# Optimization experiments

Hardware: AMD Instinct MI355X
Metric: run time of the kernel (lower is better)

Reference implementation:

```python
import jax, jax.numpy as jnp
import numpy as np
from jax import lax

T = 30        # FISTA iterations
C = 64        # number of conv filters
K = 31        # filter length
LAM = 0.1     # sparsity weight
L = 5.0       # Lipschitz constant (step size 1/L)
B, N = 32, 8192


def _HT(r, H):
    # F.conv1d(r, H): r [B,1,N], H [C,1,K] -> [B,C,N-K+1] (cross-correlation, VALID)
    return lax.conv_general_dilated(r, H, (1,), 'VALID',
                                    dimension_numbers=('NCH', 'OIH', 'NCH'))


def _Hop(x, H):
    # F.conv_transpose1d(x, H): x [B,C,M], H [C,1,K] -> [B,1,M+K-1]
    # adjoint of VALID cross-correlation = FULL conv with flipped kernel, I/O swapped
    W = jnp.transpose(jnp.flip(H, -1), (1, 0, 2))  # [1,C,K] in OIH
    return lax.conv_general_dilated(x, W, (1,), [(K - 1, K - 1)],
                                    dimension_numbers=('NCH', 'OIH', 'NCH'))


def setup_inputs() -> dict:
    key = jax.random.key(0)
    k1, k2 = jax.random.split(key)
    y = jax.random.normal(k1, (B, 1, N), dtype=jnp.float32)
    H = jax.random.normal(k2, (C, 1, K), dtype=jnp.float32)
    H = H / jnp.linalg.norm(H, axis=-1, keepdims=True)  # F.normalize(p=2, dim=-1)
    return {"y": y, "H": H}


def reference(y, H):
    enc_dim = y.shape[-1] - K + 1
    Bq = y.shape[0]
    thr = LAM / L
    x0 = jnp.zeros((Bq, C, enc_dim), dtype=y.dtype)
    init = (x0, x0, jnp.float32(1.0))  # x_old, x_tmp, s_old

    def step(carry, _):
        x_old, x_tmp, s_old = carry
        res = y - _Hop(x_tmp, H)
        x_new = jax.nn.relu(x_tmp + _HT(res, H) / L - thr)
        s_new = (1.0 + jnp.sqrt(1.0 + 4.0 * s_old * s_old)) / 2.0
        x_tmp_n = x_new + (s_old - 1.0) / s_new * (x_new - x_old)
        return (x_new, x_tmp_n, s_new), None

    (x_new, _, _), _ = lax.scan(step, init, None, length=T)
    y_hat = _Hop(x_new, H)
    return (y_hat, x_new)
```

## Files before the change

kernel.cpp:

```cpp
#include <hip/hip_runtime.h>
#include <math.h>


#define BB   32
#define CCH  64
#define KF   31
#define NN   8192
#define MM   8162
#define TT   30
#define TILE 256
#define NT   32
#define HS_P 37
#define XS_C 356
#define RACC_P 292

#define BCM ((size_t)BB * CCH * MM)
#define BN  ((size_t)BB * NN)

__device__ __forceinline__ int Fi(int i) { return i + ((i >> 5) << 2); }

__global__ __launch_bounds__(256) void step_kernel(
    const float* __restrict__ y, const float* __restrict__ Hg,
    const float* __restrict__ xA,
    float* __restrict__ xW,
    const float* __restrict__ rcur, float* __restrict__ rnext,
    float* __restrict__ rzero, float c0, float c1)
{
    __shared__ __attribute__((aligned(16))) float Hs[CCH * HS_P];
    __shared__ __attribute__((aligned(16))) float resv[320];
    __shared__ __attribute__((aligned(16))) float xs[16 * XS_C];
    __shared__ __attribute__((aligned(16))) float racc[4 * RACC_P];

    const int tid = threadIdx.x;
    const int m0  = blockIdx.x * TILE;
    const int b   = blockIdx.y;
    const size_t yb = (size_t)b * NN;

    for (int s = tid; s < CCH * HS_P; s += 256) {
        int c = s / HS_P, k = s - c * HS_P;
        Hs[s] = (k < KF) ? Hg[c * KF + k] : 0.f;
    }
    for (int i = tid; i < 288; i += 256) {
        int n = m0 + i; float v = 0.f;
        if (i < 286 && n < NN) v = y[yb + n] - rcur[yb + n];
        resv[Fi(i)] = v;
    }
    for (int s = tid; s < 16 * 64; s += 256) {
        int row = s >> 6, q = s & 63;
        int raw = (q < 32) ? q : (q + 256);
        xs[row * XS_C + Fi(raw)] = 0.f;
    }
    rzero[yb + m0 + tid] = 0.f;
    __syncthreads();

    const int wv    = tid >> 6, lane = tid & 63;
    const int cb2   = lane >> 4, lanem = lane & 15;
    const int ogi   = lane & 31, csi   = lane >> 5;
    const int ib    = ogi * 9;

    float r9[9];
    #pragma unroll
    for (int j = 0; j < 9; ++j) r9[j] = 0.f;

    #pragma unroll 1
    for (int r = 0; r < 4; ++r) {
        {
            const int c = wv * 16 + r * 4 + cb2;
            float* xrow = xs + (wv * 4 + cb2) * XS_C;
            const size_t xg = ((size_t)(b * CCH + c)) * MM;
            const float* hr = Hs + c * HS_P;
            #pragma unroll
            for (int p = 0; p < 2; ++p) {
                const int lb = p * 128 + lanem * 8;
                const int mb = m0 + lb;
                const size_t g = xg + mb;
                const bool fast = (mb + 7 < MM);
                float av[8], bv[8];
                if (fast) {
                    #pragma unroll
                    for (int j = 0; j < 8; j += 2) {
                        float2 t2 = *(const float2*)(xA + g + j);
                        av[j] = t2.x; av[j + 1] = t2.y;
                    }
                    #pragma unroll
                    for (int j = 0; j < 8; j += 2) {
                        float2 t2 = *(const float2*)(xW + g + j);
                        bv[j] = t2.x; bv[j + 1] = t2.y;
                    }
                }
                float w[16];
                #pragma unroll
                for (int q = 0; q < 4; ++q) {
                    float4 qv = *(const float4*)&resv[Fi(lb + 4 * q)];
                    w[4 * q] = qv.x; w[4 * q + 1] = qv.y;
                    w[4 * q + 2] = qv.z; w[4 * q + 3] = qv.w;
                }
                float h4[4];
                #pragma unroll
                for (int i2 = 0; i2 < 4; ++i2) h4[i2] = hr[i2];
                float acc[8];
                #pragma unroll
                for (int j = 0; j < 8; ++j) acc[j] = 0.f;
                #pragma unroll
                for (int kb = 0; kb < 32; kb += 4) {
                    float hn[4];
                    if (kb < 28) {
                        #pragma unroll
                        for (int i2 = 0; i2 < 4; ++i2) hn[i2] = hr[kb + 4 + i2];
                    }
                    float4 rq;
                    if (kb < 24) rq = *(const float4*)&resv[Fi(lb + kb + 16)];
                    #pragma unroll
                    for (int kk = 0; kk < 4; ++kk) {
                        const int k = kb + kk;
                        const float h = h4[kk];
                        #pragma unroll
                        for (int j = 0; j < 8; ++j)
                            acc[j] = fmaf(w[(k + j) & 15], h, acc[j]);
                    }
                    if (kb < 24) {
                        w[(kb + 0) & 15] = rq.x; w[(kb + 1) & 15] = rq.y;
                        w[(kb + 2) & 15] = rq.z; w[(kb + 3) & 15] = rq.w;
                    }
                    if (kb < 28) {
                        #pragma unroll
                        for (int i2 = 0; i2 < 4; ++i2) h4[i2] = hn[i2];
                    }
                }
                if (fast) {
                    float xn[8], x1[8];
                    #pragma unroll
                    for (int j = 0; j < 8; ++j) {
                        float xt = fmaf(c0, av[j] - bv[j], av[j]);
                        xn[j] = fmaxf(fmaf(acc[j], 0.2f, xt) - 0.02f, 0.f);
                        x1[j] = fmaf(c1, xn[j] - av[j], xn[j]);
                    }
                    *(float4*)&xrow[Fi(32 + lb)] =
                        make_float4(x1[0], x1[1], x1[2], x1[3]);
                    *(float4*)&xrow[Fi(32 + lb + 4)] =
                        make_float4(x1[4], x1[5], x1[6], x1[7]);
                    #pragma unroll
                    for (int j = 0; j < 8; j += 2)
                        *(float2*)(xW + g + j) = make_float2(xn[j], xn[j + 1]);
                } else {
                    #pragma unroll
                    for (int j = 0; j < 8; ++j) {
                        float x1 = 0.f;
                        if (mb + j < MM) {
                            float a = xA[g + j], b2 = xW[g + j];
                            float xt = fmaf(c0, a - b2, a);
                            float v  = fmaxf(fmaf(acc[j], 0.2f, xt) - 0.02f, 0.f);
                            xW[g + j] = v;
                            x1 = fmaf(c1, v - a, v);
                        }
                        xrow[Fi(32 + lb + j)] = x1;
                    }
                }
            }
        }

        #pragma unroll
        for (int cc = 0; cc < 2; ++cc) {
            const int cl = 2 * csi + cc;
            const float* xr = xs + (wv * 4 + cl) * XS_C;
            const float* hc = Hs + (wv * 16 + r * 4 + cl) * HS_P;
            float w[16];
            #pragma unroll
            for (int s = 0; s < 16; ++s) w[s] = xr[Fi(32 + ib - 7 + s)];
            float h4[4];
            #pragma unroll
            for (int i2 = 0; i2 < 4; ++i2) h4[i2] = hc[i2];
            #pragma unroll
            for (int kb = 0; kb < 32; kb += 4) {
                float hn[4];
                if (kb < 28) {
                    #pragma unroll
                    for (int i2 = 0; i2 < 4; ++i2) hn[i2] = hc[kb + 4 + i2];
                }
                float rv[4];
                if (kb < 24) {
                    #pragma unroll
                    for (int i2 = 0; i2 < 4; ++i2)
                        rv[i2] = xr[Fi(32 + ib - 8 - (kb + i2))];
                }
                #pragma unroll
                for (int kk = 0; kk < 4; ++kk) {
                    const int k = kb + kk;
                    const float h = h4[kk];
                    #pragma unroll
                    for (int j = 0; j < 9; ++j)
                        r9[j] = fmaf(w[(j - k + 7) & 15], h, r9[j]);
                }
                if (kb < 24) {
                    #pragma unroll
                    for (int i2 = 0; i2 < 4; ++i2)
                        w[(15 - (kb + i2)) & 15] = rv[i2];
                }
                if (kb < 28) {
                    #pragma unroll
                    for (int i2 = 0; i2 < 4; ++i2) h4[i2] = hn[i2];
                }
            }
        }
    }

    #pragma unroll
    for (int j = 0; j < 9; ++j) r9[j] += __shfl_xor(r9[j], 32);
    if (lane < 32) {
        #pragma unroll
        for (int j = 0; j < 9; ++j) racc[wv * RACC_P + ib + j] = r9[j];
    }
    __syncthreads();
    for (int i = tid; i < 286; i += 256) {
        int n = m0 + i;
        if (n < NN) {
            float s4 = racc[i] + racc[RACC_P + i] +
                       racc[2 * RACC_P + i] + racc[3 * RACC_P + i];
            atomicAdd(&rnext[yb + n], s4);
        }
    }
}

extern "C" void kernel_launch(void* const* d_in, const int* in_sizes, int n_in,
                              void* d_out, int out_size, void* d_ws, size_t ws_size,
                              hipStream_t stream) {
    const float* y  = (const float*)d_in[0];
    const float* Hg = (const float*)d_in[1];

    float* out  = (float*)d_out;
    float* yhat = out;
    float* xout = out + BN;
    float* x0w  = (float*)d_ws;
    float* r0   = x0w + BCM;
    float* r1   = r0 + BN;
    float* r2   = r1 + BN;
    float* rb[3] = {r0, r1, r2};

    hipMemsetAsync(x0w, 0, (BCM + 3 * BN) * sizeof(float), stream);
    hipMemsetAsync(out, 0, (BN + BCM) * sizeof(float), stream);

    dim3 grid(NT, BB);
    float s = 1.f, beta_prev = 0.f;
    for (int t = 0; t < TT; ++t) {
        float snew = (1.f + sqrtf(1.f + 4.f * s * s)) * 0.5f;
        float beta = (s - 1.f) / snew;
        float c1v = (t == TT - 1) ? 0.f : beta;
        float* xWt       = (t & 1) ? xout : x0w;
        const float* xAt = (t & 1) ? x0w  : xout;
        float* rnext = (t == TT - 1) ? yhat : rb[(t + 1) % 3];
        step_kernel<<<grid, 256, 0, stream>>>(y, Hg, xAt, xWt,
            rb[t % 3], rnext, rb[(t + 2) % 3], beta_prev, c1v);
        beta_prev = beta;
        s = snew;
    }
}
```

Measured before the change: 2.247 ms.

## Enlarge tile to 384, keep filter taps in registers, restructure transpose conv

The tile grows from 256 to 384 outputs per block, so the grid drops from 32 to 22 tiles per batch and the 30-tap halo overhead shrinks relative to useful work. The filter is stored in a reordered shared layout and loaded once into 32 registers per channel, so both the correlation and the transpose convolution reuse them instead of re-reading shared memory each tap. The transpose conv now has each lane compute 8 outputs for its own channel, then reduces across the four channel lanes with shuffles and accumulates into shared memory, plus a separate tail pass for the halo outputs. The cost is higher register pressure, extra shuffle and shared-memory read-modify-write traffic, and fewer blocks in flight.

```diff
diff --git a/kernel.cpp b/kernel.cpp
--- a/kernel.cpp
+++ b/kernel.cpp
@@ -8,11 +8,11 @@
 #define NN   8192
 #define MM   8162
 #define TT   30
-#define TILE 256
-#define NT   32
-#define HS_P 37
-#define XS_C 356
-#define RACC_P 292
+#define TILE 384
+#define NTI  22
+#define XS_C 500
+#define RV_N 464
+#define RP   464
 
 #define BCM ((size_t)BB * CCH * MM)
 #define BN  ((size_t)BB * NN)
@@ -26,196 +26,201 @@
     const float* __restrict__ rcur, float* __restrict__ rnext,
     float* __restrict__ rzero, float c0, float c1)
 {
-    __shared__ __attribute__((aligned(16))) float Hs[CCH * HS_P];
-    __shared__ __attribute__((aligned(16))) float resv[320];
+    __shared__ __attribute__((aligned(16))) float Hs2[2048];
+    __shared__ __attribute__((aligned(16))) float resv[RV_N];
     __shared__ __attribute__((aligned(16))) float xs[16 * XS_C];
-    __shared__ __attribute__((aligned(16))) float racc[4 * RACC_P];
+    __shared__ __attribute__((aligned(16))) float racc[4 * RP];
 
     const int tid = threadIdx.x;
     const int m0  = blockIdx.x * TILE;
     const int b   = blockIdx.y;
     const size_t yb = (size_t)b * NN;
 
-    for (int s = tid; s < CCH * HS_P; s += 256) {
-        int c = s / HS_P, k = s - c * HS_P;
-        Hs[s] = (k < KF) ? Hg[c * KF + k] : 0.f;
-    }
-    for (int i = tid; i < 288; i += 256) {
+    for (int s = tid; s < 2048; s += 256) {
+        int g = s >> 7, rem = s & 127;
+        int q = rem >> 4, sl = rem & 15;
+        int cb = sl >> 2, e = sl & 3;
+        int c = (g >> 2) * 16 + (g & 3) * 4 + cb;
+        int tap = q * 4 + e;
+        Hs2[s] = (tap < KF) ? Hg[c * KF + tap] : 0.f;
+    }
+    for (int i = tid; i < 416; i += 256) {
         int n = m0 + i; float v = 0.f;
-        if (i < 286 && n < NN) v = y[yb + n] - rcur[yb + n];
+        if (i < 414 && n < NN) v = y[yb + n] - rcur[yb + n];
         resv[Fi(i)] = v;
     }
     for (int s = tid; s < 16 * 64; s += 256) {
         int row = s >> 6, q = s & 63;
-        int raw = (q < 32) ? q : (q + 256);
+        int raw = (q < 32) ? q : (q + 384);
         xs[row * XS_C + Fi(raw)] = 0.f;
     }
-    rzero[yb + m0 + tid] = 0.f;
+    for (int s = tid; s < 4 * RP; s += 256) racc[s] = 0.f;
+    for (int i = tid; i < TILE; i += 256) {
+        int n = m0 + i;
+        if (n < NN) rzero[yb + n] = 0.f;
+    }
     __syncthreads();
 
     const int wv    = tid >> 6, lane = tid & 63;
     const int cb2   = lane >> 4, lanem = lane & 15;
-    const int ogi   = lane & 31, csi   = lane >> 5;
-    const int ib    = ogi * 9;
-
-    float r9[9];
-    #pragma unroll
-    for (int j = 0; j < 9; ++j) r9[j] = 0.f;
 
     #pragma unroll 1
     for (int r = 0; r < 4; ++r) {
+        const int c = wv * 16 + r * 4 + cb2;
+        float* xrow = xs + (wv * 4 + cb2) * XS_C;
+        const size_t xg = ((size_t)(b * CCH + c)) * MM;
+
+        float hv[32];
         {
-            const int c = wv * 16 + r * 4 + cb2;
-            float* xrow = xs + (wv * 4 + cb2) * XS_C;
-            const size_t xg = ((size_t)(b * CCH + c)) * MM;
-            const float* hr = Hs + c * HS_P;
-            #pragma unroll
-            for (int p = 0; p < 2; ++p) {
-                const int lb = p * 128 + lanem * 8;
-                const int mb = m0 + lb;
-                const size_t g = xg + mb;
-                const bool fast = (mb + 7 < MM);
-                float av[8], bv[8];
-                if (fast) {
+            const int hb = (wv * 4 + r) * 128 + cb2 * 4;
+            #pragma unroll
+            for (int q = 0; q < 8; ++q) {
+                float4 t = *(const float4*)&Hs2[hb + q * 16];
+                hv[q*4] = t.x; hv[q*4+1] = t.y; hv[q*4+2] = t.z; hv[q*4+3] = t.w;
+            }
+        }
+
+        #pragma unroll 1
+        for (int p = 0; p < 3; ++p) {
+            const int lb = p * 128 + lanem * 8;
+            const int mb = m0 + lb;
+            const size_t g = xg + mb;
+            const bool fast = (mb + 7 < MM);
+            float av[8], bv[8];
+            if (fast) {
+                #pragma unroll
+                for (int j = 0; j < 8; j += 2) {
+                    float2 t2 = *(const float2*)(xA + g + j);
+                    av[j] = t2.x; av[j + 1] = t2.y;
+                }
+                #pragma unroll
+                for (int j = 0; j < 8; j += 2) {
+                    float2 t2 = *(const float2*)(xW + g + j);
+                    bv[j] = t2.x; bv[j + 1] = t2.y;
+                }
+            }
+            float w[16];
+            #pragma unroll
+            for (int q = 0; q < 4; ++q) {
+                float4 v = *(const float4*)&resv[Fi(lb + 4 * q)];
+                w[4*q] = v.x; w[4*q+1] = v.y; w[4*q+2] = v.z; w[4*q+3] = v.w;
+            }
+            float acc[8];
+            #pragma unroll
+            for (int j = 0; j < 8; ++j) acc[j] = 0.f;
+            #pragma unroll
+            for (int kb = 0; kb < 32; kb += 4) {
+                float4 rq;
+                if (kb <= 20) rq = *(const float4*)&resv[Fi(lb + 16 + kb)];
+                #pragma unroll
+                for (int kk = 0; kk < 4; ++kk) {
+                    const float h = hv[kb + kk];
                     #pragma unroll
-                    for (int j = 0; j < 8; j += 2) {
-                        float2 t2 = *(const float2*)(xA + g + j);
-                        av[j] = t2.x; av[j + 1] = t2.y;
+                    for (int j = 0; j < 8; ++j)
+                        acc[j] = fmaf(w[(kb + kk + j) & 15], h, acc[j]);
+                }
+                if (kb <= 20) {
+                    w[kb & 15] = rq.x; w[(kb+1) & 15] = rq.y;
+                    w[(kb+2) & 15] = rq.z; w[(kb+3) & 15] = rq.w;
+                }
+            }
+            if (fast) {
+                float xn[8], x1[8];
+                #pragma unroll
+                for (int j = 0; j < 8; ++j) {
+                    float xt = fmaf(c0, av[j] - bv[j], av[j]);
+                    xn[j] = fmaxf(fmaf(acc[j], 0.2f, xt) - 0.02f, 0.f);
+                    x1[j] = fmaf(c1, xn[j] - av[j], xn[j]);
+                }
+                *(float4*)&xrow[Fi(32 + lb)] =
+                    make_float4(x1[0], x1[1], x1[2], x1[3]);
+                *(float4*)&xrow[Fi(36 + lb)] =
+                    make_float4(x1[4], x1[5], x1[6], x1[7]);
+                #pragma unroll
+                for (int j = 0; j < 8; j += 2)
+                    *(float2*)(xW + g + j) = make_float2(xn[j], xn[j + 1]);
+            } else {
+                #pragma unroll
+                for (int j = 0; j < 8; ++j) {
+                    float x1 = 0.f;
+                    if (mb + j < MM) {
+                        float a = xA[g + j], b2 = xW[g + j];
+                        float xt = fmaf(c0, a - b2, a);
+                        float v  = fmaxf(fmaf(acc[j], 0.2f, xt) - 0.02f, 0.f);
+                        xW[g + j] = v;
+                        x1 = fmaf(c1, v - a, v);
                     }
+                    xrow[Fi(32 + lb + j)] = x1;
+                }
+            }
+        }
+
+        #pragma unroll 1
+        for (int p2 = 0; p2 < 3; ++p2) {
+            const int lb = p2 * 128 + lanem * 8;
+            float w[16];
+            #pragma unroll
+            for (int q = 0; q < 4; ++q) {
+                float4 v = *(const float4*)&xrow[Fi(24 + lb + 4 * q)];
+                w[4*q] = v.x; w[4*q+1] = v.y; w[4*q+2] = v.z; w[4*q+3] = v.w;
+            }
+            float a8[8];
+            #pragma unroll
+            for (int j = 0; j < 8; ++j) a8[j] = 0.f;
+            #pragma unroll
+            for (int kb = 0; kb < 32; kb += 4) {
+                float4 rq;
+                if (kb <= 20) rq = *(const float4*)&xrow[Fi(20 + lb - kb)];
+                #pragma unroll
+                for (int kk = 0; kk < 4; ++kk) {
+                    const float h = hv[kb + kk];
                     #pragma unroll
-                    for (int j = 0; j < 8; j += 2) {
-                        float2 t2 = *(const float2*)(xW + g + j);
-                        bv[j] = t2.x; bv[j + 1] = t2.y;
-                    }
-                }
-                float w[16];
-                #pragma unroll
-                for (int q = 0; q < 4; ++q) {
-                    float4 qv = *(const float4*)&resv[Fi(lb + 4 * q)];
-                    w[4 * q] = qv.x; w[4 * q + 1] = qv.y;
-                    w[4 * q + 2] = qv.z; w[4 * q + 3] = qv.w;
-                }
-                float h4[4];
-                #pragma unroll
-                for (int i2 = 0; i2 < 4; ++i2) h4[i2] = hr[i2];
-                float acc[8];
-                #pragma unroll
-                for (int j = 0; j < 8; ++j) acc[j] = 0.f;
-                #pragma unroll
-                for (int kb = 0; kb < 32; kb += 4) {
-                    float hn[4];
-                    if (kb < 28) {
-                        #pragma unroll
-                        for (int i2 = 0; i2 < 4; ++i2) hn[i2] = hr[kb + 4 + i2];
-                    }
-                    float4 rq;
-                    if (kb < 24) rq = *(const float4*)&resv[Fi(lb + kb + 16)];
-                    #pragma unroll
-                    for (int kk = 0; kk < 4; ++kk) {
-                        const int k = kb + kk;
-                        const float h = h4[kk];
-                        #pragma unroll
-                        for (int j = 0; j < 8; ++j)
-                            acc[j] = fmaf(w[(k + j) & 15], h, acc[j]);
-                    }
-                    if (kb < 24) {
-                        w[(kb + 0) & 15] = rq.x; w[(kb + 1) & 15] = rq.y;
-                        w[(kb + 2) & 15] = rq.z; w[(kb + 3) & 15] = rq.w;
-                    }
-                    if (kb < 28) {
-                        #pragma unroll
-                        for (int i2 = 0; i2 < 4; ++i2) h4[i2] = hn[i2];
-                    }
-                }
-                if (fast) {
-                    float xn[8], x1[8];
-                    #pragma unroll
-                    for (int j = 0; j < 8; ++j) {
-                        float xt = fmaf(c0, av[j] - bv[j], av[j]);
-                        xn[j] = fmaxf(fmaf(acc[j], 0.2f, xt) - 0.02f, 0.f);
-                        x1[j] = fmaf(c1, xn[j] - av[j], xn[j]);
-                    }
-                    *(float4*)&xrow[Fi(32 + lb)] =
-                        make_float4(x1[0], x1[1], x1[2], x1[3]);
-                    *(float4*)&xrow[Fi(32 + lb + 4)] =
-                        make_float4(x1[4], x1[5], x1[6], x1[7]);
-                    #pragma unroll
-                    for (int j = 0; j < 8; j += 2)
-                        *(float2*)(xW + g + j) = make_float2(xn[j], xn[j + 1]);
-                } else {
-                    #pragma unroll
-                    for (int j = 0; j < 8; ++j) {
-                        float x1 = 0.f;
-                        if (mb + j < MM) {
-                            float a = xA[g + j], b2 = xW[g + j];
-                            float xt = fmaf(c0, a - b2, a);
-                            float v  = fmaxf(fmaf(acc[j], 0.2f, xt) - 0.02f, 0.f);
-                            xW[g + j] = v;
-                            x1 = fmaf(c1, v - a, v);
-                        }
-                        xrow[Fi(32 + lb + j)] = x1;
-                    }
-                }
-            }
-        }
-
-        #pragma unroll
-        for (int cc = 0; cc < 2; ++cc) {
-            const int cl = 2 * csi + cc;
-            const float* xr = xs + (wv * 4 + cl) * XS_C;
-            const float* hc = Hs + (wv * 16 + r * 4 + cl) * HS_P;
-            float w[16];
-            #pragma unroll
-            for (int s = 0; s < 16; ++s) w[s] = xr[Fi(32 + ib - 7 + s)];
-            float h4[4];
-            #pragma unroll
-            for (int i2 = 0; i2 < 4; ++i2) h4[i2] = hc[i2];
-            #pragma unroll
-            for (int kb = 0; kb < 32; kb += 4) {
-                float hn[4];
-                if (kb < 28) {
-                    #pragma unroll
-                    for (int i2 = 0; i2 < 4; ++i2) hn[i2] = hc[kb + 4 + i2];
-                }
-                float rv[4];
-                if (kb < 24) {
-                    #pragma unroll
-                    for (int i2 = 0; i2 < 4; ++i2)
-                        rv[i2] = xr[Fi(32 + ib - 8 - (kb + i2))];
-                }
-                #pragma unroll
-                for (int kk = 0; kk < 4; ++kk) {
-                    const int k = kb + kk;
-                    const float h = h4[kk];
-                    #pragma unroll
-                    for (int j = 0; j < 9; ++j)
-                        r9[j] = fmaf(w[(j - k + 7) & 15], h, r9[j]);
-                }
-                if (kb < 24) {
-                    #pragma unroll
-                    for (int i2 = 0; i2 < 4; ++i2)
-                        w[(15 - (kb + i2)) & 15] = rv[i2];
-                }
-                if (kb < 28) {
-                    #pragma unroll
-                    for (int i2 = 0; i2 < 4; ++i2) h4[i2] = hn[i2];
-                }
-            }
-        }
-    }
-
-    #pragma unroll
-    for (int j = 0; j < 9; ++j) r9[j] += __shfl_xor(r9[j], 32);
-    if (lane < 32) {
-        #pragma unroll
-        for (int j = 0; j < 9; ++j) racc[wv * RACC_P + ib + j] = r9[j];
-    }
+                    for (int j = 0; j < 8; ++j)
+                        a8[j] = fmaf(w[(j - kb - kk + 8) & 15], h, a8[j]);
+                }
+                if (kb <= 20) {
+                    w[(12 - kb) & 15] = rq.x; w[(13 - kb) & 15] = rq.y;
+                    w[(14 - kb) & 15] = rq.z; w[(15 - kb) & 15] = rq.w;
+                }
+            }
+            #pragma unroll
+            for (int j = 0; j < 8; ++j) {
+                a8[j] += __shfl_xor(a8[j], 16);
+                a8[j] += __shfl_xor(a8[j], 32);
+            }
+            if (cb2 == 0) {
+                #pragma unroll
+                for (int j = 0; j < 8; ++j)
+                    racc[wv * RP + Fi(lb + j)] += a8[j];
+            }
+        }
+
+        {
+            const int lbt = 384 + lanem * 2;
+            float w[33];
+            #pragma unroll
+            for (int s = 0; s < 33; ++s) w[s] = xrow[Fi(1 + lbt + s)];
+            float t0 = 0.f, t1 = 0.f;
+            #pragma unroll
+            for (int k = 0; k < KF; ++k) {
+                t0 = fmaf(w[31 - k], hv[k], t0);
+                t1 = fmaf(w[32 - k], hv[k], t1);
+            }
+            t0 += __shfl_xor(t0, 16); t0 += __shfl_xor(t0, 32);
+            t1 += __shfl_xor(t1, 16); t1 += __shfl_xor(t1, 32);
+            if (cb2 == 0) {
+                if (lbt < 414)     racc[wv * RP + Fi(lbt)]     += t0;
+                if (lbt + 1 < 414) racc[wv * RP + Fi(lbt + 1)] += t1;
+            }
+        }
+    }
+
     __syncthreads();
-    for (int i = tid; i < 286; i += 256) {
+    for (int i = tid; i < 414; i += 256) {
         int n = m0 + i;
         if (n < NN) {
-            float s4 = racc[i] + racc[RACC_P + i] +
-                       racc[2 * RACC_P + i] + racc[3 * RACC_P + i];
+            int f = Fi(i);
+            float s4 = racc[f] + racc[RP + f] + racc[2 * RP + f] + racc[3 * RP + f];
             atomicAdd(&rnext[yb + n], s4);
         }
     }
@@ -239,7 +244,7 @@
     hipMemsetAsync(x0w, 0, (BCM + 3 * BN) * sizeof(float), stream);
     hipMemsetAsync(out, 0, (BN + BCM) * sizeof(float), stream);
 
-    dim3 grid(NT, BB);
+    dim3 grid(NTI, BB);
     float s = 1.f, beta_prev = 0.f;
     for (int t = 0; t < TT; ++t) {
         float snew = (1.f + sqrtf(1.f + 4.f * s * s)) * 0.5f;
```

Result: faster. 1.916 ms (-14.7%).
